# Performance work log

Hardware: AMD Instinct MI355X
Metric: run time of the kernel (lower is better)

The kernel has to match this reference:

```python
import jax, jax.numpy as jnp
import numpy as np

B, L, HID, NH = 8, 384, 512, 8
DH = HID // NH
MAX_SEQ_LEN = 384  # module's max_seq_len; pe has 2*MAX_SEQ_LEN rows


def setup_inputs() -> dict:
    key = jax.random.key(0)
    ks = jax.random.split(key, 16)
    s = 0.02
    inp = {
        "key": jax.random.normal(ks[0], (B, L, HID), jnp.float32),
        "query": jax.random.normal(ks[1], (B, L, HID), jnp.float32),
        "value": jax.random.normal(ks[2], (B, L, HID), jnp.float32),
        "seq_len": jnp.maximum(
            jax.random.randint(ks[3], (B,), L // 2, L + 1), 0
        ).at[0].set(L),  # ensure max(seq_len) == L
        "pe": jax.random.normal(ks[4], (2 * MAX_SEQ_LEN, HID), jnp.float32) * s,
        "Wk": jax.random.normal(ks[5], (HID, HID), jnp.float32) * s,
        "bk": jnp.zeros((HID,), jnp.float32),
        "Wq": jax.random.normal(ks[6], (HID, HID), jnp.float32) * s,
        "bq": jnp.zeros((HID,), jnp.float32),
        "Wv": jax.random.normal(ks[7], (HID, HID), jnp.float32) * s,
        "bv": jnp.zeros((HID,), jnp.float32),
        "Wr": jax.random.normal(ks[8], (HID, HID), jnp.float32) * s,
        "br": jnp.zeros((HID,), jnp.float32),
        "u_bias": jax.random.normal(ks[9], (NH, DH), jnp.float32) * s,
        "v_bias": jax.random.normal(ks[10], (NH, DH), jnp.float32) * s,
        "Wf": jax.random.normal(ks[11], (HID, HID), jnp.float32) * s,
        "bf": jnp.zeros((HID,), jnp.float32),
    }
    return inp


def reference(key, query, value, seq_len, pe, Wk, bk, Wq, bq, Wv, bv, Wr, br,
              u_bias, v_bias, Wf, bf):
    b, l, hid = key.shape
    # relative distance matrix: rel[i, j] = j - i
    idx = jnp.arange(l)
    rel = idx[None, :] - idx[:, None]                       # [L, L]
    rpe = pe[rel + MAX_SEQ_LEN]                             # [L, L, HID] gather

    k = (key @ Wk.T + bk).reshape(b, l, NH, DH).transpose(0, 2, 1, 3)    # [b,h,L,d]
    q = (query @ Wq.T + bq).reshape(b, l, NH, DH).transpose(0, 2, 1, 3)
    v = (value @ Wv.T + bv).reshape(b, l, NH, DH).transpose(0, 2, 1, 3)
    r = (rpe @ Wr.T + br).reshape(l, l, NH, DH)             # [L,L,h,d]

    A = jnp.einsum("bhid,bhjd->bhij", q, k)
    Bt = jnp.einsum("bhid,ijhd->bhij", q, r)
    C = jnp.einsum("hd,bhjd->bhj", u_bias, k)[:, :, None, :]  # broadcast over i
    D = jnp.einsum("ijhd,hd->hij", r, v_bias)[None]            # broadcast over b

    score = (A + Bt + C + D) / jnp.sqrt(jnp.float32(DH))
    mask = (idx[None, :] < seq_len[:, None])[:, None, None, :]  # [b,1,1,L]
    score = jnp.where(mask, score, jnp.float32(-1e15))
    attn = jax.nn.softmax(score, axis=-1)

    out = jnp.einsum("bhij,bhjd->bhid", attn, v)
    out = out.transpose(0, 2, 1, 3).reshape(b, l, hid)
    out = out @ Wf.T + bf  # ff_final
    return out
```

## Files before the change

### kernel.cpp

```cpp
#include <hip/hip_runtime.h>
#include <hip/hip_bf16.h>

typedef short v8s __attribute__((ext_vector_type(8)));
typedef float v4f __attribute__((ext_vector_type(4)));
typedef float float4v __attribute__((ext_vector_type(4)));
typedef unsigned short u16x4 __attribute__((ext_vector_type(4)));

#define BB 8
#define LL 384
#define HIDD 512
#define NHH 8
#define DHH 64
#define PP 768
#define BL (BB*LL)

using bf16 = __hip_bfloat16;

__device__ __forceinline__ v8s ld8(const bf16* p){
  return *reinterpret_cast<const v8s*>(p);
}

struct Ptrs { const void* p[16]; };

#define CAST_GROUPS 1606528

__global__ __launch_bounds__(256)
void cast_inputs(Ptrs ptrs, bf16* __restrict__ dst){
  __shared__ int smode;
  int tid = threadIdx.x;
  if (tid < 64){
    const unsigned int* key_raw = (const unsigned int*)ptrs.p[0];
    int huge = 0, zeros = 0;
    #pragma unroll
    for (int c = 0; c < 4; c++){
      unsigned int lo = key_raw[tid*4 + c] & 0xFFFFu;
      if (((lo >> 7) & 0xFF) >= 0x90u) huge++;
      if (lo == 0u) zeros++;
    }
    #pragma unroll
    for (int off = 32; off; off >>= 1){
      huge  += __shfl_xor(huge,  off);
      zeros += __shfl_xor(zeros, off);
    }
    if (tid == 0) smode = (huge > 8 || zeros > 200) ? 1 : 0;
  }
  __syncthreads();
  int mode = smode;

  const int start[17] = {0, 393216, 786432, 1179648, 1277952, 1343488, 1343616,
                         1409152, 1409280, 1474816, 1474944, 1540480, 1540608,
                         1540736, 1540864, 1606400, 1606528};
  int g = blockIdx.x*256 + tid;
  if (g >= CAST_GROUPS) return;
  int s = 0;
  #pragma unroll
  for (int i = 0; i < 16; i++) if (g >= start[i+1]) s = i+1;
  int local = g - start[s];
  u16x4 outv;
  if (mode){
    const float4v* src = (const float4v*)ptrs.p[s];
    float4v f = src[local];
    #pragma unroll
    for (int i = 0; i < 4; i++){
      bf16 h = __float2bfloat16(f[i]);
      outv[i] = *reinterpret_cast<unsigned short*>(&h);
    }
  } else {
    const u16x4* src = (const u16x4*)ptrs.p[s];
    outv = src[local];
  }
  *reinterpret_cast<u16x4*>(dst + (long)g*4) = outv;
}

__global__ void zero_out(float* __restrict__ out, int n){
  int i = blockIdx.x*256 + threadIdx.x;
  if (i < n) out[i] = 0.f;
}

__global__ __launch_bounds__(256)
void proj_gemm(const bf16* __restrict__ arena, bf16* __restrict__ outbase,
               bf16* __restrict__ vT, float* __restrict__ uk, float* __restrict__ rd)
{
  __shared__ alignas(16) bf16 ldsA[128*72];
  __shared__ alignas(16) bf16 ldsB[64*72];
  __shared__ float part[4*128];

  int z = blockIdx.z;
  if (z == 3 && blockIdx.y >= 6) return;
  const bf16* A    = arena + (long)z*1572864;
  const bf16* Bw   = arena + 5111808 + (long)z*262656;
  const bf16* bias = arena + 5373952 + (long)z*262656;

  int tid  = threadIdx.x;
  int lane = tid & 63, w = tid >> 6;
  int l16  = lane & 15, quad = lane >> 4;
  long g0  = (long)blockIdx.y * 128;
  int h    = blockIdx.x;
  int mloc = (w >> 1) * 64;
  int nloc = (w & 1) * 32;

  v4f acc[4][2] = {};
  for (int kk = 0; kk < HIDD; kk += 64){
    __syncthreads();
    #pragma unroll
    for (int c4 = 0; c4 < 4; c4++){
      int id = tid + c4*256;
      int row = id >> 3, c = id & 7;
      v8s v = ld8(A + (g0 + row)*HIDD + kk + c*8);
      *(v8s*)&ldsA[row*72 + c*8] = v;
    }
    #pragma unroll
    for (int c2 = 0; c2 < 2; c2++){
      int id = tid + c2*256;
      int row = id >> 3, c = id & 7;
      v8s v = ld8(Bw + (long)(h*64 + row)*HIDD + kk + c*8);
      *(v8s*)&ldsB[row*72 + c*8] = v;
    }
    __syncthreads();
    #pragma unroll
    for (int kq = 0; kq < 2; kq++){
      v8s af[4], bfr[2];
      #pragma unroll
      for (int ti = 0; ti < 4; ti++)
        af[ti] = *(const v8s*)&ldsA[(mloc + ti*16 + l16)*72 + kq*32 + quad*8];
      #pragma unroll
      for (int tj = 0; tj < 2; tj++)
        bfr[tj] = *(const v8s*)&ldsB[(nloc + tj*16 + l16)*72 + kq*32 + quad*8];
      #pragma unroll
      for (int ti = 0; ti < 4; ti++)
        #pragma unroll
        for (int tj = 0; tj < 2; tj++)
          acc[ti][tj] = __builtin_amdgcn_mfma_f32_16x16x32_bf16(af[ti], bfr[tj], acc[ti][tj], 0,0,0);
    }
  }

  if (z != 2){
    bf16* C = outbase + (long)z*1572864;
    #pragma unroll
    for (int ti = 0; ti < 4; ti++)
      #pragma unroll
      for (int tj = 0; tj < 2; tj++){
        int col = h*64 + nloc + tj*16 + l16;
        float bv = __bfloat162float(bias[col]);
        #pragma unroll
        for (int r = 0; r < 4; r++){
          long row = g0 + mloc + ti*16 + quad*4 + r;
          C[row*HIDD + col] = __float2bfloat16(acc[ti][tj][r] + bv);
        }
      }
  }

  if (z != 1){
    __syncthreads();
    bf16* tileT = ldsA;
    #pragma unroll
    for (int ti = 0; ti < 4; ti++)
      #pragma unroll
      for (int tj = 0; tj < 2; tj++){
        int lcol = nloc + tj*16 + l16;
        float bv = __bfloat162float(bias[h*64 + lcol]);
        #pragma unroll
        for (int r = 0; r < 4; r++){
          int lrow = mloc + ti*16 + quad*4 + r;
          tileT[lcol*132 + lrow] = __float2bfloat16(acc[ti][tj][r] + bv);
        }
      }
    __syncthreads();

    if (z == 2){
      int b = (int)(g0/LL), j0 = (int)(g0%LL);
      int d = tid >> 2, jc = (tid & 3)*32;
      #pragma unroll
      for (int s = 0; s < 4; s++){
        v8s v = *(const v8s*)&tileT[d*132 + jc + s*8];
        *(v8s*)&vT[((long)b*HIDD + h*64 + d)*LL + j0 + jc + s*8] = v;
      }
    } else {
      const bf16* vec = arena + (z == 0 ? 6162432 : 6162944) + h*64;
      int row2 = tid & 63;
      int pi   = tid >> 6;
      float s0 = 0.f, s1 = 0.f;
      #pragma unroll
      for (int dd = 0; dd < 16; dd++){
        int d = pi*16 + dd;
        float uvd = __bfloat162float(vec[d]);
        s0 += __bfloat162float(tileT[d*132 + row2])      * uvd;
        s1 += __bfloat162float(tileT[d*132 + row2 + 64]) * uvd;
      }
      part[pi*128 + row2]      = s0;
      part[pi*128 + row2 + 64] = s1;
      __syncthreads();
      if (tid < 128){
        float tot = part[tid] + part[128+tid] + part[256+tid] + part[384+tid];
        if (z == 0){
          int b = (int)(g0/LL), j0 = (int)(g0%LL);
          uk[((long)b*NHH + h)*LL + j0 + tid] = tot;
        } else {
          rd[h*PP + (int)g0 + tid] = tot;
        }
      }
    }
  }
}

__global__ __launch_bounds__(256)
void gemm_final(const bf16* __restrict__ A, const bf16* __restrict__ Bw,
                const bf16* __restrict__ bias, float* __restrict__ C)
{
  int lane = threadIdx.x & 63;
  int w    = threadIdx.x >> 6;
  int l16  = lane & 15, quad = lane >> 4;
  int mbase = blockIdx.y*64 + (w>>1)*32;
  int nbase = blockIdx.x*64 + (w&1)*32;

  v4f acc[2][2] = {};
  #pragma unroll 4
  for (int kk = 0; kk < HIDD; kk += 32){
    v8s a0 = ld8(A + (long)(mbase      + l16)*HIDD + kk + quad*8);
    v8s a1 = ld8(A + (long)(mbase + 16 + l16)*HIDD + kk + quad*8);
    v8s b0 = ld8(Bw + (long)(nbase      + l16)*HIDD + kk + quad*8);
    v8s b1 = ld8(Bw + (long)(nbase + 16 + l16)*HIDD + kk + quad*8);
    acc[0][0] = __builtin_amdgcn_mfma_f32_16x16x32_bf16(a0,b0,acc[0][0],0,0,0);
    acc[0][1] = __builtin_amdgcn_mfma_f32_16x16x32_bf16(a0,b1,acc[0][1],0,0,0);
    acc[1][0] = __builtin_amdgcn_mfma_f32_16x16x32_bf16(a1,b0,acc[1][0],0,0,0);
    acc[1][1] = __builtin_amdgcn_mfma_f32_16x16x32_bf16(a1,b1,acc[1][1],0,0,0);
  }
  for (int ti = 0; ti < 2; ti++){
    for (int tj = 0; tj < 2; tj++){
      int col = nbase + tj*16 + l16;
      float bv = __bfloat162float(bias[col]);
      #pragma unroll
      for (int r = 0; r < 4; r++){
        int row = mbase + ti*16 + quad*4 + r;
        C[(long)row*HIDD + col] = acc[ti][tj][r] + bv;
      }
    }
  }
}

#define BTS_S 404
#define S_S   397
#define PB_S  408

__global__ __launch_bounds__(256)
void attn_kernel(const bf16* __restrict__ qb, const bf16* __restrict__ kb,
                 const bf16* __restrict__ vT, const bf16* __restrict__ rproj,
                 const float* __restrict__ uk, const float* __restrict__ rd,
                 const unsigned int* __restrict__ sraw, bf16* __restrict__ attn_out)
{
  __shared__ alignas(16) bf16  Bts[16*BTS_S];
  __shared__ alignas(16) float S[16*S_S];
  __shared__ alignas(16) bf16  Pb[16*PB_S];
  __shared__ float rsum[16];
  __shared__ int s_slen;

  int i0 = blockIdx.x*16;
  int h  = blockIdx.y, b = blockIdx.z;
  int lane = threadIdx.x & 63, wave = threadIdx.x >> 6;
  int l16 = lane & 15, quad = lane >> 4;
  int p0 = 369 - i0;

  if (threadIdx.x == 0){
    bool i64 = true;
    for (int bb = 0; bb < BB; bb++){
      unsigned int w0 = sraw[2*bb], w1 = sraw[2*bb+1];
      if (!(w1 == 0u && w0 >= 1u && w0 < 100000u)) { i64 = false; break; }
    }
    unsigned int w = i64 ? sraw[2*b] : sraw[b];
    int v = (w < 100000u) ? (int)w : (int)(__uint_as_float(w) + 0.5f);
    s_slen = min(max(v, 0), LL);
  }

  const bf16* qp = qb + (long)(b*LL + i0 + l16)*HIDD + h*DHH;
  v8s aq0 = ld8(qp + quad*8);
  v8s aq1 = ld8(qp + 32 + quad*8);

  #pragma unroll 2
  for (int nt = wave; nt < 25; nt += 4){
    int pbase = p0 + nt*16;
    int prow = min(pbase + l16, PP-1);
    const bf16* rp = rproj + (long)prow*HIDD + h*DHH;
    v8s b0 = ld8(rp + quad*8);
    v8s b1 = ld8(rp + 32 + quad*8);
    v4f acc = {};
    acc = __builtin_amdgcn_mfma_f32_16x16x32_bf16(aq0, b0, acc, 0,0,0);
    acc = __builtin_amdgcn_mfma_f32_16x16x32_bf16(aq1, b1, acc, 0,0,0);
    float rdv = rd[h*PP + prow];
    #pragma unroll
    for (int r = 0; r < 4; r++)
      Bts[(quad*4 + r)*BTS_S + nt*16 + l16] = __float2bfloat16(acc[r] + rdv);
  }
  __syncthreads();
  int slen = s_slen;

  #pragma unroll 2
  for (int jt = wave; jt < 24; jt += 4){
    int j0 = jt*16;
    const bf16* kp = kb + (long)(b*LL + j0 + l16)*HIDD + h*DHH;
    v8s b0 = ld8(kp + quad*8);
    v8s b1 = ld8(kp + 32 + quad*8);
    v4f acc = {};
    acc = __builtin_amdgcn_mfma_f32_16x16x32_bf16(aq0, b0, acc, 0,0,0);
    acc = __builtin_amdgcn_mfma_f32_16x16x32_bf16(aq1, b1, acc, 0,0,0);
    int j = j0 + l16;
    float c_add = uk[(b*NHH + h)*LL + j];
    #pragma unroll
    for (int r = 0; r < 4; r++){
      int il = quad*4 + r;
      float bt = __bfloat162float(Bts[il*BTS_S + (j - il + 15)]);
      float s = (acc[r] + bt + c_add) * 0.125f;
      if (j >= slen) s = -1e15f;
      S[il*S_S + j] = s;
    }
  }
  __syncthreads();

  for (int rr = 0; rr < 4; rr++){
    int row = wave*4 + rr;
    float vals[6];
    float m = -3.0e38f;
    #pragma unroll
    for (int t = 0; t < 6; t++){
      vals[t] = S[row*S_S + lane + t*64];
      m = fmaxf(m, vals[t]);
    }
    #pragma unroll
    for (int off = 32; off; off >>= 1) m = fmaxf(m, __shfl_xor(m, off));
    float sum = 0.f;
    #pragma unroll
    for (int t = 0; t < 6; t++){
      float e = __expf(vals[t] - m);
      sum += e;
      Pb[row*PB_S + lane + t*64] = __float2bfloat16(e);
    }
    #pragma unroll
    for (int off = 32; off; off >>= 1) sum += __shfl_xor(sum, off);
    if (lane == 0) rsum[row] = sum;
  }
  __syncthreads();

  {
    int d0 = wave*16;
    v4f o = {};
    const bf16* vp = vT + ((long)(b*NHH + h)*DHH + d0 + l16)*LL;
    #pragma unroll 4
    for (int kt = 0; kt < 12; kt++){
      v8s a  = *reinterpret_cast<const v8s*>(&Pb[l16*PB_S + kt*32 + quad*8]);
      v8s bb = ld8(vp + kt*32 + quad*8);
      o = __builtin_amdgcn_mfma_f32_16x16x32_bf16(a, bb, o, 0,0,0);
    }
    #pragma unroll
    for (int r = 0; r < 4; r++){
      int il = quad*4 + r;
      float val = o[r] / rsum[il];
      attn_out[(long)(b*LL + i0 + il)*HIDD + h*DHH + d0 + l16] = __float2bfloat16(val);
    }
  }
}

extern "C" void kernel_launch(void* const* d_in, const int* in_sizes, int n_in,
                              void* d_out, int out_size, void* d_ws, size_t ws_size,
                              hipStream_t stream)
{
  float* out = (float*)d_out;

  const int expect[17] = {1572864, 1572864, 1572864, 8, 393216,
                          262144, 512, 262144, 512, 262144, 512, 262144, 512,
                          512, 512, 262144, 512};
  bool ok = (n_in == 17);
  if (ok) for (int i = 0; i < 17; i++) if (in_sizes[i] != expect[i]) { ok = false; break; }
  if (!ok){
    zero_out<<<dim3((out_size + 255)/256), dim3(256), 0, stream>>>(out, out_size);
    return;
  }

  char* ws = (char*)d_ws;
  bf16*  cast   = (bf16*)(ws);
  bf16*  kb     = (bf16*)(ws + 12852224);
  bf16*  qb     = (bf16*)(ws + 15997952);
  bf16*  vT     = (bf16*)(ws + 19143680);
  bf16*  rproj  = (bf16*)(ws + 22289408);
  bf16*  attn_o = (bf16*)(ws + 25435136);
  float* uk     = (float*)(ws + 28580864);
  float* rd     = (float*)(ws + 28679168);
  (void)ws_size;

  const bf16* Wfc = cast + 6163456;
  const bf16* bfc = cast + 6425600;

  Ptrs ptrs;
  {
    int k = 0;
    for (int i = 0; i < 17; i++){ if (i == 3) continue; ptrs.p[k++] = d_in[i]; }
  }

  dim3 blk(256);
  cast_inputs<<<dim3((CAST_GROUPS + 255)/256), blk, 0, stream>>>(ptrs, cast);
  proj_gemm<<<dim3(8, 24, 4), blk, 0, stream>>>(cast, kb, vT, uk, rd);
  attn_kernel<<<dim3(LL/16, NHH, BB), blk, 0, stream>>>(
      qb, kb, vT, rproj, uk, rd, (const unsigned int*)d_in[3], attn_o);
  gemm_final<<<dim3(8, 48, 1), blk, 0, stream>>>(attn_o, Wfc, bfc, out);
}
```

Before: 170.6 us.

## Fuse fp32-to-bf16 input cast into projection and final GEMM loads

Removes the separate cast_inputs kernel that converted every input to bf16 in a workspace arena. The projection and final GEMMs now read the original input buffers directly and convert fp32 to bf16 while loading, using a per-block dtype detection on the key input. This drops one launch and the write and re-read of the casted copy. The cost is scalar fp32 loads and conversions inside the GEMM load loops, and every block repeats the detection step.

```diff
diff --git a/kernel.cpp b/kernel.cpp
--- a/kernel.cpp
+++ b/kernel.cpp
@@ -4,7 +4,6 @@
 typedef short v8s __attribute__((ext_vector_type(8)));
 typedef float v4f __attribute__((ext_vector_type(4)));
 typedef float float4v __attribute__((ext_vector_type(4)));
-typedef unsigned short u16x4 __attribute__((ext_vector_type(4)));
 
 #define BB 8
 #define LL 384
@@ -19,17 +18,24 @@
 __device__ __forceinline__ v8s ld8(const bf16* p){
   return *reinterpret_cast<const v8s*>(p);
 }
-
-struct Ptrs { const void* p[16]; };
-
-#define CAST_GROUPS 1606528
-
-__global__ __launch_bounds__(256)
-void cast_inputs(Ptrs ptrs, bf16* __restrict__ dst){
-  __shared__ int smode;
-  int tid = threadIdx.x;
+__device__ __forceinline__ v8s cvt8(const float* p){
+  v8s r;
+  #pragma unroll
+  for (int i = 0; i < 8; i++){
+    bf16 h = __float2bfloat16(p[i]);
+    r[i] = *reinterpret_cast<short*>(&h);
+  }
+  return r;
+}
+__device__ __forceinline__ v8s load8(const void* base, long elem, int mode){
+  if (mode) return cvt8((const float*)base + elem);
+  return *((const v8s*)((const bf16*)base + elem));
+}
+__device__ __forceinline__ float ld1(const void* p, int i, int mode){
+  return mode ? ((const float*)p)[i] : __bfloat162float(((const bf16*)p)[i]);
+}
+__device__ __forceinline__ int detect_mode(const unsigned int* key_raw, int tid, int* smode){
   if (tid < 64){
-    const unsigned int* key_raw = (const unsigned int*)ptrs.p[0];
     int huge = 0, zeros = 0;
     #pragma unroll
     for (int c = 0; c < 4; c++){
@@ -42,34 +48,10 @@
       huge  += __shfl_xor(huge,  off);
       zeros += __shfl_xor(zeros, off);
     }
-    if (tid == 0) smode = (huge > 8 || zeros > 200) ? 1 : 0;
+    if (tid == 0) *smode = (huge > 8 || zeros > 200) ? 1 : 0;
   }
   __syncthreads();
-  int mode = smode;
-
-  const int start[17] = {0, 393216, 786432, 1179648, 1277952, 1343488, 1343616,
-                         1409152, 1409280, 1474816, 1474944, 1540480, 1540608,
-                         1540736, 1540864, 1606400, 1606528};
-  int g = blockIdx.x*256 + tid;
-  if (g >= CAST_GROUPS) return;
-  int s = 0;
-  #pragma unroll
-  for (int i = 0; i < 16; i++) if (g >= start[i+1]) s = i+1;
-  int local = g - start[s];
-  u16x4 outv;
-  if (mode){
-    const float4v* src = (const float4v*)ptrs.p[s];
-    float4v f = src[local];
-    #pragma unroll
-    for (int i = 0; i < 4; i++){
-      bf16 h = __float2bfloat16(f[i]);
-      outv[i] = *reinterpret_cast<unsigned short*>(&h);
-    }
-  } else {
-    const u16x4* src = (const u16x4*)ptrs.p[s];
-    outv = src[local];
-  }
-  *reinterpret_cast<u16x4*>(dst + (long)g*4) = outv;
+  return *smode;
 }
 
 __global__ void zero_out(float* __restrict__ out, int n){
@@ -77,21 +59,33 @@
   if (i < n) out[i] = 0.f;
 }
 
+struct ProjPtrs {
+  const void* A[4];
+  const void* W[4];
+  const void* bias[4];
+  const void* ub;
+  const void* vbias;
+  const unsigned int* key_raw;
+};
+
 __global__ __launch_bounds__(256)
-void proj_gemm(const bf16* __restrict__ arena, bf16* __restrict__ outbase,
+void proj_gemm(ProjPtrs P, bf16* __restrict__ outbase,
                bf16* __restrict__ vT, float* __restrict__ uk, float* __restrict__ rd)
 {
   __shared__ alignas(16) bf16 ldsA[128*72];
   __shared__ alignas(16) bf16 ldsB[64*72];
   __shared__ float part[4*128];
+  __shared__ int smode;
+
+  int tid  = threadIdx.x;
+  int mode = detect_mode(P.key_raw, tid, &smode);
 
   int z = blockIdx.z;
   if (z == 3 && blockIdx.y >= 6) return;
-  const bf16* A    = arena + (long)z*1572864;
-  const bf16* Bw   = arena + 5111808 + (long)z*262656;
-  const bf16* bias = arena + 5373952 + (long)z*262656;
-
-  int tid  = threadIdx.x;
+  const void* A    = P.A[z];
+  const void* Bw   = P.W[z];
+  const void* bias = P.bias[z];
+
   int lane = tid & 63, w = tid >> 6;
   int l16  = lane & 15, quad = lane >> 4;
   long g0  = (long)blockIdx.y * 128;
@@ -106,15 +100,13 @@
     for (int c4 = 0; c4 < 4; c4++){
       int id = tid + c4*256;
       int row = id >> 3, c = id & 7;
-      v8s v = ld8(A + (g0 + row)*HIDD + kk + c*8);
-      *(v8s*)&ldsA[row*72 + c*8] = v;
+      *(v8s*)&ldsA[row*72 + c*8] = load8(A, (g0 + row)*HIDD + kk + c*8, mode);
     }
     #pragma unroll
     for (int c2 = 0; c2 < 2; c2++){
       int id = tid + c2*256;
       int row = id >> 3, c = id & 7;
-      v8s v = ld8(Bw + (long)(h*64 + row)*HIDD + kk + c*8);
-      *(v8s*)&ldsB[row*72 + c*8] = v;
+      *(v8s*)&ldsB[row*72 + c*8] = load8(Bw, (long)(h*64 + row)*HIDD + kk + c*8, mode);
     }
     __syncthreads();
     #pragma unroll
@@ -141,7 +133,7 @@
       #pragma unroll
       for (int tj = 0; tj < 2; tj++){
         int col = h*64 + nloc + tj*16 + l16;
-        float bv = __bfloat162float(bias[col]);
+        float bv = ld1(bias, col, mode);
         #pragma unroll
         for (int r = 0; r < 4; r++){
           long row = g0 + mloc + ti*16 + quad*4 + r;
@@ -158,7 +150,7 @@
       #pragma unroll
       for (int tj = 0; tj < 2; tj++){
         int lcol = nloc + tj*16 + l16;
-        float bv = __bfloat162float(bias[h*64 + lcol]);
+        float bv = ld1(bias, h*64 + lcol, mode);
         #pragma unroll
         for (int r = 0; r < 4; r++){
           int lrow = mloc + ti*16 + quad*4 + r;
@@ -176,14 +168,14 @@
         *(v8s*)&vT[((long)b*HIDD + h*64 + d)*LL + j0 + jc + s*8] = v;
       }
     } else {
-      const bf16* vec = arena + (z == 0 ? 6162432 : 6162944) + h*64;
+      const void* vec = (z == 0) ? P.ub : P.vbias;
       int row2 = tid & 63;
       int pi   = tid >> 6;
       float s0 = 0.f, s1 = 0.f;
       #pragma unroll
       for (int dd = 0; dd < 16; dd++){
         int d = pi*16 + dd;
-        float uvd = __bfloat162float(vec[d]);
+        float uvd = ld1(vec, h*64 + d, mode);
         s0 += __bfloat162float(tileT[d*132 + row2])      * uvd;
         s1 += __bfloat162float(tileT[d*132 + row2 + 64]) * uvd;
       }
@@ -204,11 +196,16 @@
 }
 
 __global__ __launch_bounds__(256)
-void gemm_final(const bf16* __restrict__ A, const bf16* __restrict__ Bw,
-                const bf16* __restrict__ bias, float* __restrict__ C)
+void gemm_final(const bf16* __restrict__ A, const void* __restrict__ Bw,
+                const void* __restrict__ bias, const unsigned int* __restrict__ key_raw,
+                float* __restrict__ C)
 {
-  int lane = threadIdx.x & 63;
-  int w    = threadIdx.x >> 6;
+  __shared__ int smode;
+  int tid  = threadIdx.x;
+  int mode = detect_mode(key_raw, tid, &smode);
+
+  int lane = tid & 63;
+  int w    = tid >> 6;
   int l16  = lane & 15, quad = lane >> 4;
   int mbase = blockIdx.y*64 + (w>>1)*32;
   int nbase = blockIdx.x*64 + (w&1)*32;
@@ -218,8 +215,8 @@
   for (int kk = 0; kk < HIDD; kk += 32){
     v8s a0 = ld8(A + (long)(mbase      + l16)*HIDD + kk + quad*8);
     v8s a1 = ld8(A + (long)(mbase + 16 + l16)*HIDD + kk + quad*8);
-    v8s b0 = ld8(Bw + (long)(nbase      + l16)*HIDD + kk + quad*8);
-    v8s b1 = ld8(Bw + (long)(nbase + 16 + l16)*HIDD + kk + quad*8);
+    v8s b0 = load8(Bw, (long)(nbase      + l16)*HIDD + kk + quad*8, mode);
+    v8s b1 = load8(Bw, (long)(nbase + 16 + l16)*HIDD + kk + quad*8, mode);
     acc[0][0] = __builtin_amdgcn_mfma_f32_16x16x32_bf16(a0,b0,acc[0][0],0,0,0);
     acc[0][1] = __builtin_amdgcn_mfma_f32_16x16x32_bf16(a0,b1,acc[0][1],0,0,0);
     acc[1][0] = __builtin_amdgcn_mfma_f32_16x16x32_bf16(a1,b0,acc[1][0],0,0,0);
@@ -228,7 +225,7 @@
   for (int ti = 0; ti < 2; ti++){
     for (int tj = 0; tj < 2; tj++){
       int col = nbase + tj*16 + l16;
-      float bv = __bfloat162float(bias[col]);
+      float bv = ld1(bias, col, mode);
       #pragma unroll
       for (int r = 0; r < 4; r++){
         int row = mbase + ti*16 + quad*4 + r;
@@ -375,29 +372,26 @@
   }
 
   char* ws = (char*)d_ws;
-  bf16*  cast   = (bf16*)(ws);
-  bf16*  kb     = (bf16*)(ws + 12852224);
-  bf16*  qb     = (bf16*)(ws + 15997952);
-  bf16*  vT     = (bf16*)(ws + 19143680);
-  bf16*  rproj  = (bf16*)(ws + 22289408);
-  bf16*  attn_o = (bf16*)(ws + 25435136);
-  float* uk     = (float*)(ws + 28580864);
-  float* rd     = (float*)(ws + 28679168);
+  bf16*  kb     = (bf16*)(ws);
+  bf16*  qb     = (bf16*)(ws +  3145728);
+  bf16*  vT     = (bf16*)(ws +  6291456);
+  bf16*  rproj  = (bf16*)(ws +  9437184);
+  bf16*  attn_o = (bf16*)(ws + 12582912);
+  float* uk     = (float*)(ws + 15728640);
+  float* rd     = (float*)(ws + 15826944);
   (void)ws_size;
 
-  const bf16* Wfc = cast + 6163456;
-  const bf16* bfc = cast + 6425600;
-
-  Ptrs ptrs;
-  {
-    int k = 0;
-    for (int i = 0; i < 17; i++){ if (i == 3) continue; ptrs.p[k++] = d_in[i]; }
-  }
+  ProjPtrs P;
+  P.A[0] = d_in[0];  P.A[1] = d_in[1];  P.A[2] = d_in[2];  P.A[3] = d_in[4];
+  P.W[0] = d_in[5];  P.W[1] = d_in[7];  P.W[2] = d_in[9];  P.W[3] = d_in[11];
+  P.bias[0] = d_in[6]; P.bias[1] = d_in[8]; P.bias[2] = d_in[10]; P.bias[3] = d_in[12];
+  P.ub = d_in[13]; P.vbias = d_in[14];
+  P.key_raw = (const unsigned int*)d_in[0];
 
   dim3 blk(256);
-  cast_inputs<<<dim3((CAST_GROUPS + 255)/256), blk, 0, stream>>>(ptrs, cast);
-  proj_gemm<<<dim3(8, 24, 4), blk, 0, stream>>>(cast, kb, vT, uk, rd);
+  proj_gemm<<<dim3(8, 24, 4), blk, 0, stream>>>(P, kb, vT, uk, rd);
   attn_kernel<<<dim3(LL/16, NHH, BB), blk, 0, stream>>>(
       qb, kb, vT, rproj, uk, rd, (const unsigned int*)d_in[3], attn_o);
-  gemm_final<<<dim3(8, 48, 1), blk, 0, stream>>>(attn_o, Wfc, bfc, out);
-}
+  gemm_final<<<dim3(8, 48, 1), blk, 0, stream>>>(
+      attn_o, d_in[15], d_in[16], (const unsigned int*)d_in[0], out);
+}
```

Result: slower. 184.1 us (+7.9%).

## Tile final GEMM through LDS with larger blocks; prefetch V fragments before softmax

Applied to the files above, without the earlier changes.

The final projection GEMM now stages 128x64 A tiles and 64x64 weight tiles in shared memory, with each wave computing a 64x32 output. Previously every wave loaded its operands straight from global memory. This cuts redundant global loads, and the grid is halved to match the larger tile. Separately, the attention kernel loads the V fragments into registers before the softmax phase, so their latency overlaps with the softmax work. The cost is higher register pressure and more LDS use, which may lower occupancy.

```diff
diff --git a/kernel.cpp b/kernel.cpp
--- a/kernel.cpp
+++ b/kernel.cpp
@@ -207,35 +207,64 @@
 void gemm_final(const bf16* __restrict__ A, const bf16* __restrict__ Bw,
                 const bf16* __restrict__ bias, float* __restrict__ C)
 {
-  int lane = threadIdx.x & 63;
-  int w    = threadIdx.x >> 6;
+  __shared__ alignas(16) bf16 ldsA[128*72];
+  __shared__ alignas(16) bf16 ldsB[64*72];
+
+  int tid  = threadIdx.x;
+  int lane = tid & 63, w = tid >> 6;
   int l16  = lane & 15, quad = lane >> 4;
-  int mbase = blockIdx.y*64 + (w>>1)*32;
-  int nbase = blockIdx.x*64 + (w&1)*32;
-
-  v4f acc[2][2] = {};
-  #pragma unroll 4
-  for (int kk = 0; kk < HIDD; kk += 32){
-    v8s a0 = ld8(A + (long)(mbase      + l16)*HIDD + kk + quad*8);
-    v8s a1 = ld8(A + (long)(mbase + 16 + l16)*HIDD + kk + quad*8);
-    v8s b0 = ld8(Bw + (long)(nbase      + l16)*HIDD + kk + quad*8);
-    v8s b1 = ld8(Bw + (long)(nbase + 16 + l16)*HIDD + kk + quad*8);
-    acc[0][0] = __builtin_amdgcn_mfma_f32_16x16x32_bf16(a0,b0,acc[0][0],0,0,0);
-    acc[0][1] = __builtin_amdgcn_mfma_f32_16x16x32_bf16(a0,b1,acc[0][1],0,0,0);
-    acc[1][0] = __builtin_amdgcn_mfma_f32_16x16x32_bf16(a1,b0,acc[1][0],0,0,0);
-    acc[1][1] = __builtin_amdgcn_mfma_f32_16x16x32_bf16(a1,b1,acc[1][1],0,0,0);
-  }
-  for (int ti = 0; ti < 2; ti++){
+  long g0  = (long)blockIdx.y * 128;
+  int h    = blockIdx.x;
+  int mloc = (w >> 1) * 64;
+  int nloc = (w & 1) * 32;
+
+  v4f acc[4][2] = {};
+  for (int kk = 0; kk < HIDD; kk += 64){
+    __syncthreads();
+    #pragma unroll
+    for (int c4 = 0; c4 < 4; c4++){
+      int id = tid + c4*256;
+      int row = id >> 3, c = id & 7;
+      v8s v = ld8(A + (g0 + row)*HIDD + kk + c*8);
+      *(v8s*)&ldsA[row*72 + c*8] = v;
+    }
+    #pragma unroll
+    for (int c2 = 0; c2 < 2; c2++){
+      int id = tid + c2*256;
+      int row = id >> 3, c = id & 7;
+      v8s v = ld8(Bw + (long)(h*64 + row)*HIDD + kk + c*8);
+      *(v8s*)&ldsB[row*72 + c*8] = v;
+    }
+    __syncthreads();
+    #pragma unroll
+    for (int kq = 0; kq < 2; kq++){
+      v8s af[4], bfr[2];
+      #pragma unroll
+      for (int ti = 0; ti < 4; ti++)
+        af[ti] = *(const v8s*)&ldsA[(mloc + ti*16 + l16)*72 + kq*32 + quad*8];
+      #pragma unroll
+      for (int tj = 0; tj < 2; tj++)
+        bfr[tj] = *(const v8s*)&ldsB[(nloc + tj*16 + l16)*72 + kq*32 + quad*8];
+      #pragma unroll
+      for (int ti = 0; ti < 4; ti++)
+        #pragma unroll
+        for (int tj = 0; tj < 2; tj++)
+          acc[ti][tj] = __builtin_amdgcn_mfma_f32_16x16x32_bf16(af[ti], bfr[tj], acc[ti][tj], 0,0,0);
+    }
+  }
+
+  #pragma unroll
+  for (int ti = 0; ti < 4; ti++)
+    #pragma unroll
     for (int tj = 0; tj < 2; tj++){
-      int col = nbase + tj*16 + l16;
+      int col = h*64 + nloc + tj*16 + l16;
       float bv = __bfloat162float(bias[col]);
       #pragma unroll
       for (int r = 0; r < 4; r++){
-        int row = mbase + ti*16 + quad*4 + r;
-        C[(long)row*HIDD + col] = acc[ti][tj][r] + bv;
-      }
-    }
-  }
+        long row = g0 + mloc + ti*16 + quad*4 + r;
+        C[row*HIDD + col] = acc[ti][tj][r] + bv;
+      }
+    }
 }
 
 #define BTS_S 404
@@ -315,6 +344,12 @@
   }
   __syncthreads();
 
+  int d0 = wave*16;
+  const bf16* vp = vT + ((long)(b*NHH + h)*DHH + d0 + l16)*LL;
+  v8s vfrag[12];
+  #pragma unroll
+  for (int kt = 0; kt < 12; kt++) vfrag[kt] = ld8(vp + kt*32 + quad*8);
+
   for (int rr = 0; rr < 4; rr++){
     int row = wave*4 + rr;
     float vals[6];
@@ -340,14 +375,11 @@
   __syncthreads();
 
   {
-    int d0 = wave*16;
     v4f o = {};
-    const bf16* vp = vT + ((long)(b*NHH + h)*DHH + d0 + l16)*LL;
     #pragma unroll 4
     for (int kt = 0; kt < 12; kt++){
-      v8s a  = *reinterpret_cast<const v8s*>(&Pb[l16*PB_S + kt*32 + quad*8]);
-      v8s bb = ld8(vp + kt*32 + quad*8);
-      o = __builtin_amdgcn_mfma_f32_16x16x32_bf16(a, bb, o, 0,0,0);
+      v8s a = *reinterpret_cast<const v8s*>(&Pb[l16*PB_S + kt*32 + quad*8]);
+      o = __builtin_amdgcn_mfma_f32_16x16x32_bf16(a, vfrag[kt], o, 0,0,0);
     }
     #pragma unroll
     for (int r = 0; r < 4; r++){
@@ -399,5 +431,5 @@
   proj_gemm<<<dim3(8, 24, 4), blk, 0, stream>>>(cast, kb, vT, uk, rd);
   attn_kernel<<<dim3(LL/16, NHH, BB), blk, 0, stream>>>(
       qb, kb, vT, rproj, uk, rd, (const unsigned int*)d_in[3], attn_o);
-  gemm_final<<<dim3(8, 48, 1), blk, 0, stream>>>(attn_o, Wfc, bfc, out);
-}
+  gemm_final<<<dim3(8, 24, 1), blk, 0, stream>>>(attn_o, Wfc, bfc, out);
+}
```

New measurement: 181.0 us. +6.1%, slower.
